# Kernel optimization log

Hardware: AMD Instinct MI355X
Metric: run time of the kernel (lower is better)

## Reference

```python
import jax, jax.numpy as jnp
import numpy as np
jax.config.update('jax_enable_x64', True)

N = 64
NX = N * N
BATCH = 32
EPS = 0.1
N_ITER = 25
SCHUR_REG = 1e-9
BIG = 1e10


def _constraints(group_ids, exposure):
    """Build shared equality system A z = b (doubly-stochastic + fairness row).
    Matches torch code which uses A = A[0] (first batch element only)."""
    ROW = jnp.kron(jnp.eye(N, dtype=jnp.float64), jnp.ones((1, N), dtype=jnp.float64))  # row sums
    COL = jnp.kron(jnp.ones((1, N), dtype=jnp.float64), jnp.eye(N, dtype=jnp.float64))  # col sums
    g = group_ids[0].astype(jnp.float64)                       # [N]
    f = g / g.sum() - (1.0 - g) / (1.0 - g).sum()              # group contrast
    fair = (f[:, None] * exposure.astype(jnp.float64)[None, :]).reshape(1, NX)  # entry i*N+j = f_i * expo_j
    A = jnp.concatenate([ROW, COL, fair], axis=0)              # [2N+1, NX]
    b = jnp.concatenate([jnp.ones(2 * N, dtype=jnp.float64), jnp.zeros(1, dtype=jnp.float64)])
    return A, b


def _solve_qp(p, A, b):
    """Batched primal-dual interior point for min 0.5*eps*||z||^2 + p'z
    s.t. A z = b, 0 <= z <= 1. G=[-I;I] structure is exploited: G'DG is diagonal,
    so each Newton step reduces to a small [neq,neq] Schur solve (as in qpth)."""
    B, nx = p.shape
    neq = A.shape[0]
    m = 2 * nx
    h = jnp.concatenate([jnp.zeros(nx, dtype=p.dtype), jnp.ones(nx, dtype=p.dtype)])
    eye_neq = jnp.eye(neq, dtype=p.dtype)

    def step(carry, _):
        z, y, s, lam = carry
        s1, s2 = s[:, :nx], s[:, nx:]
        l1, l2 = lam[:, :nx], lam[:, nx:]
        Gz = jnp.concatenate([-z, z], axis=1)
        r_dual = EPS * z + p + y @ A + (-l1 + l2)          # Qz + p + A'y + G'lam
        r_eq = z @ A.T - b                                  # A z - b
        r_ineq = Gz + s - h                                 # G z + s - h
        mu = jnp.sum(s * lam, axis=1, keepdims=True) / m
        r_cent = lam * s - 0.1 * mu                         # sigma = 0.1 centering
        tmp = (lam * r_ineq - r_cent) / s                   # [B, 2nx]
        rhs_z = -(r_dual + (-tmp[:, :nx] + tmp[:, nx:]))
        invD = 1.0 / (EPS + l1 / s1 + l2 / s2)              # (Q + G'DG)^{-1} diagonal
        S = jnp.einsum('ik,bk,jk->bij', A, invD, A) + SCHUR_REG * eye_neq
        rhs_y = (rhs_z * invD) @ A.T + r_eq
        dy = jnp.linalg.solve(S, rhs_y[..., None])[..., 0]
        dz = (rhs_z - dy @ A) * invD
        ds = -r_ineq - jnp.concatenate([-dz, dz], axis=1)
        dlam = (-r_cent - lam * ds) / s
        # fraction-to-boundary step length (grad-safe division)
        den_s = jnp.where(ds < 0, ds, -1.0)
        den_l = jnp.where(dlam < 0, dlam, -1.0)
        a_s = jnp.where(ds < 0, -s / den_s, BIG).min(axis=1)
        a_l = jnp.where(dlam < 0, -lam / den_l, BIG).min(axis=1)
        alpha = jnp.minimum(1.0, 0.99 * jnp.minimum(a_s, a_l))[:, None]
        return (z + alpha * dz, y + alpha * dy, s + alpha * ds, lam + alpha * dlam), None

    init = (jnp.zeros_like(p), jnp.zeros((B, neq), p.dtype),
            jnp.ones((B, m), p.dtype), jnp.ones((B, m), p.dtype))
    (z, _, _, _), _ = jax.lax.scan(step, init, None, length=N_ITER)
    return z


def setup_inputs() -> dict:
    key = jax.random.key(0)
    k1, k2 = jax.random.split(key)
    x = jax.random.normal(k1, (BATCH, NX), dtype=jnp.float32)
    gid = jax.random.randint(k2, (BATCH, N), 0, 2).astype(jnp.float32)
    # guarantee both groups present (avoid division by zero in f)
    gid = gid.at[:, 0].set(1.0).at[:, 1].set(0.0)
    exposure = (1.0 / jnp.log2(jnp.arange(N, dtype=jnp.float32) + 2.0))  # position_bias_vector[:N]
    return {"x": x, "group_ids": gid, "exposure": exposure}


def reference(x, group_ids, exposure):
    A, b = _constraints(group_ids, exposure)
    p = x.astype(jnp.float64)
    z = _solve_qp(p, A, b)
    return z.reshape(-1, N, N).astype(jnp.float32)
```

## Files before the change

kernel.cpp:

```cpp
#include <hip/hip_runtime.h>
#include <math.h>

#define NN    64
#define NXX   4096
#define NT    512
#define NCH   8
#define NITER 25
#define EPSQ  0.1
#define SREG  1e-9
#define BIGV  1e10

__device__ __forceinline__ double wsum(double v) {
#pragma unroll
  for (int m = 32; m > 0; m >>= 1) v += __shfl_xor(v, m, 64);
  return v;
}
__device__ __forceinline__ double wmin(double v) {
#pragma unroll
  for (int m = 32; m > 0; m >>= 1) v = fmin(v, __shfl_xor(v, m, 64));
  return v;
}
__device__ __forceinline__ double wmax(double v) {
#pragma unroll
  for (int m = 32; m > 0; m >>= 1) v = fmax(v, __shfl_xor(v, m, 64));
  return v;
}

__global__ __launch_bounds__(NT, 2)
void ipm_kernel(const float* __restrict__ xin, const float* __restrict__ gidin,
                const float* __restrict__ expin, float* __restrict__ outp)
{
  const int b    = blockIdx.x;
  const int tid  = threadIdx.x;
  const int lane = tid & 63;
  const int w    = tid >> 6;

  __shared__ double DnT[64][65];
  __shared__ double Mg[64][67];
  __shared__ double Pbuf[16][52];
  __shared__ double Binv[16][18];
  __shared__ double cpZ[8][64], cpA[8][64], cpB[8][64], cpC[8][64];
  __shared__ double rhs1[64], rhs2v[64];
  __shared__ double Rhv[64], Ruv[64], ccv[64], wvv[64];
  __shared__ double usv[64], rsv[64], uvv[64], mw0[64];
  __shared__ double ddv[64];
  __shared__ double yav[64], ydv[64];
  __shared__ double fvec[64], evec[64];
  __shared__ double wpFz[8], wpMu[8], wpQ[8], wpFg[8], wpS[8], wpL[8];
  __shared__ double scal[8];

  if (tid < 64) {
    fvec[tid] = (double)gidin[tid];
    evec[tid] = (double)expin[tid];
    yav[tid] = 0.0; ydv[tid] = 0.0;
  }
  if (tid == 0) scal[6] = 0.0;
  __syncthreads();
  if (tid == 0) {
    double gs = 0.0;
    for (int i = 0; i < 64; ++i) gs += fvec[i];
    scal[7] = gs;
  }
  __syncthreads();
  if (tid < 64) {
    double g = fvec[tid], gs = scal[7];
    fvec[tid] = g / gs - (1.0 - g) / (64.0 - gs);
  }
  __syncthreads();

  double p[NCH], z[NCH], s1[NCH], s2[NCH], l1[NCH], l2[NCH], fe[NCH];
  const double ev = evec[lane];
#pragma unroll
  for (int k = 0; k < NCH; ++k) {
    int e = tid + NT * k;
    p[k]  = (double)xin[(size_t)b * NXX + e];
    z[k] = 0.0; s1[k] = 1.0; s2[k] = 1.0; l1[k] = 1.0; l2[k] = 1.0;
    fe[k] = fvec[w + 8 * k] * ev;
  }

  for (int iter = 0; iter < NITER; ++iter) {
    double rq1[NCH];
    double cz = 0.0, fz = 0.0, msl = 0.0;
#pragma unroll
    for (int k = 0; k < NCH; ++k) {
      rq1[k] = wsum(z[k]) - 1.0;
      cz  += z[k];
      fz  += fe[k] * z[k];
      msl += s1[k] * l1[k] + s2[k] * l2[k];
    }
    cpZ[w][lane] = cz;
    {
      double a = wsum(fz), c = wsum(msl);
      if (lane == 0) { wpFz[w] = a; wpMu[w] = c; }
    }
    __syncthreads();

    double mu8 = 0.0;
#pragma unroll
    for (int q = 0; q < 8; ++q) mu8 += wpMu[q];
    const double mu01 = 0.1 * (mu8 / 8192.0);
    const double yt   = scal[6];
    double dinv[NCH], rz[NCH], is1[NCH], is2[NCH];
    double cD = 0.0, cfD = 0.0, cg = 0.0, qac = 0.0, fgac = 0.0;
#pragma unroll
    for (int k = 0; k < NCH; ++k) {
      int i = w + 8 * k;
      is1[k] = 1.0 / s1[k];  is2[k] = 1.0 / s2[k];
      double D = 1.0 / (EPSQ + l1[k] * is1[k] + l2[k] * is2[k]);
      dinv[k] = D;
      double rd  = EPSQ * z[k] + p[k] + (yav[i] + ydv[lane] + yt * fe[k]) + (l2[k] - l1[k]);
      double tt1 = (mu01 - l1[k] * z[k]) * is1[k];
      double tt2 = (l2[k] * (z[k] - 1.0) + mu01) * is2[k];
      double r = -(rd - tt1 + tt2);
      rz[k] = r;
      double g = r * D;
      double sD  = wsum(D);
      double sED = wsum(ev * D);
      double sg  = wsum(g);
      double Rh  = sD + SREG;
      if (lane == 0) {
        Rhv[i]  = Rh;
        Ruv[i]  = sED;
        rhs1[i] = sg + rq1[k];
      }
      DnT[lane][i] = D * rsqrt(Rh);
      cD  += D;  cfD += fvec[i] * D;  cg += g;
      qac += fe[k] * fe[k] * D;
      fgac += fe[k] * g;
    }
    cpA[w][lane] = cD; cpB[w][lane] = cfD; cpC[w][lane] = cg;
    {
      double a = wsum(qac), c = wsum(fgac);
      if (lane == 0) { wpQ[w] = a; wpFg[w] = c; }
    }
    __syncthreads();

    if (tid < 64) {
      double sZ = 0.0, sA = 0.0, sB = 0.0, sC = 0.0;
#pragma unroll
      for (int q = 0; q < 8; ++q) {
        sZ += cpZ[q][tid]; sA += cpA[q][tid]; sB += cpB[q][tid]; sC += cpC[q][tid];
      }
      ccv[tid]   = sA;
      wvv[tid]   = evec[tid] * sB;
      rhs2v[tid] = sC + sZ - 1.0;
      double ir  = rsqrt(Rhv[tid]);
      double u   = fvec[tid] * Ruv[tid];
      uvv[tid] = u;
      usv[tid] = u * ir;
      rsv[tid] = rhs1[tid] * ir;
    }
    __syncthreads();

    {
      const int r0 = (tid >> 5) << 2;
      const int c0 = (tid & 31) << 1;
      double m00=0.0,m01=0.0,m10=0.0,m11=0.0,m20=0.0,m21=0.0,m30=0.0,m31=0.0;
#pragma unroll 4
      for (int i = 0; i < 64; ++i) {
        double a0 = DnT[r0+0][i], a1 = DnT[r0+1][i];
        double a2 = DnT[r0+2][i], a3 = DnT[r0+3][i];
        double b0v = DnT[c0+0][i], b1v = DnT[c0+1][i];
        m00 += a0*b0v; m01 += a0*b1v;
        m10 += a1*b0v; m11 += a1*b1v;
        m20 += a2*b0v; m21 += a2*b1v;
        m30 += a3*b0v; m31 += a3*b1v;
      }
      Mg[r0+0][c0+0] = ((r0+0)==(c0+0) ? ccv[r0+0]+SREG : 0.0) - m00;
      Mg[r0+0][c0+1] = ((r0+0)==(c0+1) ? ccv[r0+0]+SREG : 0.0) - m01;
      Mg[r0+1][c0+0] = ((r0+1)==(c0+0) ? ccv[r0+1]+SREG : 0.0) - m10;
      Mg[r0+1][c0+1] = ((r0+1)==(c0+1) ? ccv[r0+1]+SREG : 0.0) - m11;
      Mg[r0+2][c0+0] = ((r0+2)==(c0+0) ? ccv[r0+2]+SREG : 0.0) - m20;
      Mg[r0+2][c0+1] = ((r0+2)==(c0+1) ? ccv[r0+2]+SREG : 0.0) - m21;
      Mg[r0+3][c0+0] = ((r0+3)==(c0+0) ? ccv[r0+3]+SREG : 0.0) - m30;
      Mg[r0+3][c0+1] = ((r0+3)==(c0+1) ? ccv[r0+3]+SREG : 0.0) - m31;

      int d = 16 * w + (lane >> 2);
      int j = d & 63;
      int cc = d >> 6;
      int iq = (lane & 3) * 16;
      double acc = 0.0;
#pragma unroll
      for (int i = 0; i < 16; ++i) {
        double vv = cc ? usv[iq + i] : rsv[iq + i];
        acc += DnT[j][iq + i] * vv;
      }
      acc += __shfl_xor(acc, 1, 64);
      acc += __shfl_xor(acc, 2, 64);
      if ((lane & 3) == 0) {
        if (cc == 0) Mg[j][64] = rhs2v[j] - acc;
        else { double vv2 = wvv[j] - acc; Mg[j][65] = vv2; mw0[j] = vv2; }
      }
    }
    __syncthreads();

#pragma unroll
    for (int pk = 0; pk < 4; ++pk) {
      const int k0   = 16 * pk;
      const int rest = 66 - k0 - 16;

      if (w == 0) {
        const int r = lane >> 2, q = lane & 3;
        double Brow[4];
#pragma unroll
        for (int e = 0; e < 4; ++e) Brow[e] = Mg[k0 + r][k0 + ((e << 2) | q)];
#pragma unroll
        for (int t = 0; t < 16; ++t) {
          const int et = t >> 2, qt = t & 3;
          double pm = __shfl(Brow[et], (r << 2) | qt, 64);
          double pv = __shfl(Brow[et], (t << 2) | qt, 64);
          double pr0 = __shfl(Brow[0], (t << 2) | q, 64);
          double pr1 = __shfl(Brow[1], (t << 2) | q, 64);
          double pr2 = __shfl(Brow[2], (t << 2) | q, 64);
          double pr3 = __shfl(Brow[3], (t << 2) | q, 64);
          double ip = 1.0 / pv;
          double ps0 = pr0 * ip, ps1 = pr1 * ip, ps2 = pr2 * ip, ps3 = pr3 * ip;
          if (r == t) {
            Brow[0] = ps0; Brow[1] = ps1; Brow[2] = ps2; Brow[3] = ps3;
            if (q == qt) Brow[et] = ip;
          } else {
            Brow[0] -= pm * ps0; Brow[1] -= pm * ps1;
            Brow[2] -= pm * ps2; Brow[3] -= pm * ps3;
            if (q == qt) Brow[et] = -pm * ip;
          }
        }
#pragma unroll
        for (int e = 0; e < 4; ++e) Binv[r][(e << 2) | q] = Brow[e];
      }
      __syncthreads();

      for (int o = tid; o < 16 * rest; o += NT) {
        int t = o / rest, c = o - t * rest;
        double acc = 0.0;
#pragma unroll
        for (int s = 0; s < 16; ++s) acc += Binv[t][s] * Mg[k0 + s][k0 + 16 + c];
        Pbuf[t][c] = acc;
      }
      __syncthreads();

      for (int o = tid; o < 48 * rest; o += NT) {
        int rr = o / rest, c = o - rr * rest;
        int r = rr < k0 ? rr : rr + 16;
        double acc = Mg[r][k0 + 16 + c];
#pragma unroll
        for (int t = 0; t < 16; ++t) acc -= Mg[r][k0 + t] * Pbuf[t][c];
        Mg[r][k0 + 16 + c] = acc;
      }
      for (int o = tid; o < 16 * rest; o += NT) {
        int t = o / rest, c = o - t * rest;
        Mg[k0 + t][k0 + 16 + c] = Pbuf[t][c];
      }
      __syncthreads();
    }

    if (w == 0) {
      double qsum = 0.0, fg = 0.0, fzs = 0.0;
#pragma unroll
      for (int q = 0; q < 8; ++q) { qsum += wpQ[q]; fg += wpFg[q]; fzs += wpFz[q]; }
      double h1 = Mg[lane][64], h2 = Mg[lane][65];
      double a1 = wsum(usv[lane] * usv[lane]);
      double a2 = wsum(usv[lane] * rsv[lane]);
      double a3 = wsum(mw0[lane] * h1);
      double a4 = wsum(mw0[lane] * h2);
      double qp  = qsum + SREG - a1;
      double r3p = (fg + fzs) - a2;
      double tloc = (r3p - a3) / (qp - a4);
      ddv[lane] = h1 - tloc * h2;
      if (lane == 0) scal[4] = tloc;
    }
    __syncthreads();

    const double tf = scal[4];
    double dar[NCH];
    double bs = 0.0;
    double rl = BIGV;
#pragma unroll
    for (int k = 0; k < NCH; ++k) {
      int i = w + 8 * k;
      double rdot = wsum(dinv[k] * ddv[lane]);
      double dv = (rhs1[i] - rdot - uvv[i] * tf) / Rhv[i];
      dar[k] = dv;
      double d   = (rz[k] - (dv + ddv[lane] + tf * fe[k])) * dinv[k];
      double ds1 = d - (s1[k] - z[k]);
      double ds2 = -(z[k] + s2[k] - 1.0) - d;
      bs = fmax(bs, fmax(-ds1 * is1[k], -ds2 * is2[k]));
      double dl1 = (-(l1[k] * s1[k] - mu01) - l1[k] * ds1) * is1[k];
      double dl2 = (-(l2[k] * s2[k] - mu01) - l2[k] * ds2) * is2[k];
      if (dl1 < 0.0) rl = fmin(rl, -l1[k] / dl1);
      if (dl2 < 0.0) rl = fmin(rl, -l2[k] / dl2);
    }
    bs = wmax(bs);
    rl = wmin(rl);
    if (lane == 0) { wpS[w] = bs; wpL[w] = rl; }
    __syncthreads();
    if (tid == 0) {
      double bm = wpS[0], rm = wpL[0];
      for (int q = 1; q < 8; ++q) { bm = fmax(bm, wpS[q]); rm = fmin(rm, wpL[q]); }
      double a_s = bm > 0.0 ? 1.0 / bm : BIGV;
      scal[5] = fmin(1.0, 0.99 * fmin(a_s, rm));
    }
    __syncthreads();

    const double al = scal[5];
#pragma unroll
    for (int k = 0; k < NCH; ++k) {
      double d   = (rz[k] - (dar[k] + ddv[lane] + tf * fe[k])) * dinv[k];
      double ds1 = d - (s1[k] - z[k]);
      double ds2 = -(z[k] + s2[k] - 1.0) - d;
      double dl1 = (-(l1[k] * s1[k] - mu01) - l1[k] * ds1) * is1[k];
      double dl2 = (-(l2[k] * s2[k] - mu01) - l2[k] * ds2) * is2[k];
      z[k]  += al * d;
      s1[k] += al * ds1;
      s2[k] += al * ds2;
      l1[k] += al * dl1;
      l2[k] += al * dl2;
      if (lane == 0) yav[w + 8 * k] += al * dar[k];
    }
    if (tid < 64) ydv[tid] += al * ddv[tid];
    if (tid == 0) scal[6] += al * tf;
  }

#pragma unroll
  for (int k = 0; k < NCH; ++k) {
    int e = tid + NT * k;
    outp[(size_t)b * NXX + e] = (float)z[k];
  }
}

extern "C" void kernel_launch(void* const* d_in, const int* in_sizes, int n_in,
                              void* d_out, int out_size, void* d_ws, size_t ws_size,
                              hipStream_t stream)
{
  const float* x   = (const float*)d_in[0];
  const float* gid = (const float*)d_in[1];
  const float* ex  = (const float*)d_in[2];
  float* out = (float*)d_out;
  int nb = in_sizes[0] / NXX;
  hipLaunchKernelGGL(ipm_kernel, dim3(nb), dim3(NT), 0, stream, x, gid, ex, out);
}
```

Before: 1.471 ms.

## Exploit Schur symmetry, overlap block inversion with trailing update, drop barriers

The Gram product is now computed only for upper-triangle tiles, and the lower triangle is mirrored afterward. Warp 0 inverts the next 16x16 pivot block using a Newton-refined hardware reciprocal, while the other warps update the remaining trailing matrix. This removes a barrier-separated inversion phase in each of the first three panel steps. The step-length and t-scalar computations are done redundantly in every warp instead of going through shared memory, which removes two more block barriers per iteration. The trade-offs are extra index arithmetic (sqrt-based pair decoding), load imbalance between warp 0 and the others, and slightly different reciprocal rounding.

```diff
diff --git a/kernel.cpp b/kernel.cpp
--- a/kernel.cpp
+++ b/kernel.cpp
@@ -26,6 +26,45 @@
   return v;
 }
 
+#define F1_INVERT(K0)                                                         \
+  {                                                                           \
+    const int r_ = lane >> 2, q_ = lane & 3;                                  \
+    double Brow[4];                                                           \
+    _Pragma("unroll")                                                         \
+    for (int e = 0; e < 4; ++e) Brow[e] = Mg[(K0) + r_][(K0) + ((e << 2) | q_)]; \
+    _Pragma("unroll")                                                         \
+    for (int t = 0; t < 16; ++t) {                                            \
+      const int et = t >> 2, qt = t & 3;                                      \
+      double pm  = __shfl(Brow[et], (r_ << 2) | qt, 64);                      \
+      double pv  = __shfl(Brow[et], (t << 2) | qt, 64);                       \
+      double pr0 = __shfl(Brow[0], (t << 2) | q_, 64);                        \
+      double pr1 = __shfl(Brow[1], (t << 2) | q_, 64);                        \
+      double pr2 = __shfl(Brow[2], (t << 2) | q_, 64);                        \
+      double pr3 = __shfl(Brow[3], (t << 2) | q_, 64);                        \
+      double ip = __builtin_amdgcn_rcp(pv);                                   \
+      ip = ip * (2.0 - pv * ip);                                              \
+      ip = ip * (2.0 - pv * ip);                                              \
+      double ps0 = pr0 * ip, ps1 = pr1 * ip, ps2 = pr2 * ip, ps3 = pr3 * ip;  \
+      if (r_ == t) {                                                          \
+        Brow[0] = ps0; Brow[1] = ps1; Brow[2] = ps2; Brow[3] = ps3;           \
+        if (q_ == qt) Brow[et] = ip;                                          \
+      } else {                                                                \
+        Brow[0] -= pm * ps0; Brow[1] -= pm * ps1;                             \
+        Brow[2] -= pm * ps2; Brow[3] -= pm * ps3;                             \
+        if (q_ == qt) Brow[et] = -pm * ip;                                    \
+      }                                                                       \
+    }                                                                         \
+    _Pragma("unroll")                                                         \
+    for (int e = 0; e < 4; ++e) Binv[r_][(e << 2) | q_] = Brow[e];            \
+  }
+
+__device__ __forceinline__ void pair_jl(int idx, int& j, int& l) {
+  j = (int)((1.0 + sqrt(8.0 * (double)idx + 1.0)) * 0.5);
+  while (j * (j - 1) / 2 > idx) --j;
+  while ((j + 1) * j / 2 <= idx) ++j;
+  l = idx - j * (j - 1) / 2;
+}
+
 __global__ __launch_bounds__(NT, 2)
 void ipm_kernel(const float* __restrict__ xin, const float* __restrict__ gidin,
                 const float* __restrict__ expin, float* __restrict__ outp)
@@ -43,7 +82,6 @@
   __shared__ double rhs1[64], rhs2v[64];
   __shared__ double Rhv[64], Ruv[64], ccv[64], wvv[64];
   __shared__ double usv[64], rsv[64], uvv[64], mw0[64];
-  __shared__ double ddv[64];
   __shared__ double yav[64], ydv[64];
   __shared__ double fvec[64], evec[64];
   __shared__ double wpFz[8], wpMu[8], wpQ[8], wpFg[8], wpS[8], wpL[8];
@@ -152,9 +190,12 @@
     }
     __syncthreads();
 
-    {
-      const int r0 = (tid >> 5) << 2;
-      const int c0 = (tid & 31) << 1;
+    if (tid < 272) {
+      int R = 0;
+#pragma unroll
+      for (int r = 1; r < 16; ++r) if (tid >= r * (33 - r)) R = r;
+      const int C  = 2 * R + (tid - R * (33 - R));
+      const int r0 = R << 2, c0 = C << 1;
       double m00=0.0,m01=0.0,m10=0.0,m11=0.0,m20=0.0,m21=0.0,m30=0.0,m31=0.0;
 #pragma unroll 4
       for (int i = 0; i < 64; ++i) {
@@ -174,22 +215,33 @@
       Mg[r0+2][c0+1] = ((r0+2)==(c0+1) ? ccv[r0+2]+SREG : 0.0) - m21;
       Mg[r0+3][c0+0] = ((r0+3)==(c0+0) ? ccv[r0+3]+SREG : 0.0) - m30;
       Mg[r0+3][c0+1] = ((r0+3)==(c0+1) ? ccv[r0+3]+SREG : 0.0) - m31;
-
-      int d = 16 * w + (lane >> 2);
-      int j = d & 63;
-      int cc = d >> 6;
-      int iq = (lane & 3) * 16;
+    } else if (tid < 400) {
+      const int d = tid - 272;
+      const int j = d & 63, cc = d >> 6;
       double acc = 0.0;
-#pragma unroll
-      for (int i = 0; i < 16; ++i) {
-        double vv = cc ? usv[iq + i] : rsv[iq + i];
-        acc += DnT[j][iq + i] * vv;
-      }
-      acc += __shfl_xor(acc, 1, 64);
-      acc += __shfl_xor(acc, 2, 64);
-      if ((lane & 3) == 0) {
-        if (cc == 0) Mg[j][64] = rhs2v[j] - acc;
-        else { double vv2 = wvv[j] - acc; Mg[j][65] = vv2; mw0[j] = vv2; }
+#pragma unroll 8
+      for (int i = 0; i < 64; ++i) {
+        double vv = cc ? usv[i] : rsv[i];
+        acc += DnT[j][i] * vv;
+      }
+      if (cc == 0) Mg[j][64] = rhs2v[j] - acc;
+      else { double vv2 = wvv[j] - acc; Mg[j][65] = vv2; mw0[j] = vv2; }
+    }
+    __syncthreads();
+
+    if (w == 0) {
+#pragma unroll
+      for (int e = 0; e < 2; ++e) {
+        int idx = 2 * lane + e;
+        if (idx < 120) { int j, l; pair_jl(idx, j, l); Mg[j][l] = Mg[l][j]; }
+      }
+      F1_INVERT(0);
+    } else {
+      const int wtid = tid - 64;
+#pragma unroll
+      for (int r = 0; r < 5; ++r) {
+        int idx = 120 + wtid + 448 * r;
+        if (idx < 2016) { int j, l; pair_jl(idx, j, l); Mg[j][l] = Mg[l][j]; }
       }
     }
     __syncthreads();
@@ -197,37 +249,7 @@
 #pragma unroll
     for (int pk = 0; pk < 4; ++pk) {
       const int k0   = 16 * pk;
-      const int rest = 66 - k0 - 16;
-
-      if (w == 0) {
-        const int r = lane >> 2, q = lane & 3;
-        double Brow[4];
-#pragma unroll
-        for (int e = 0; e < 4; ++e) Brow[e] = Mg[k0 + r][k0 + ((e << 2) | q)];
-#pragma unroll
-        for (int t = 0; t < 16; ++t) {
-          const int et = t >> 2, qt = t & 3;
-          double pm = __shfl(Brow[et], (r << 2) | qt, 64);
-          double pv = __shfl(Brow[et], (t << 2) | qt, 64);
-          double pr0 = __shfl(Brow[0], (t << 2) | q, 64);
-          double pr1 = __shfl(Brow[1], (t << 2) | q, 64);
-          double pr2 = __shfl(Brow[2], (t << 2) | q, 64);
-          double pr3 = __shfl(Brow[3], (t << 2) | q, 64);
-          double ip = 1.0 / pv;
-          double ps0 = pr0 * ip, ps1 = pr1 * ip, ps2 = pr2 * ip, ps3 = pr3 * ip;
-          if (r == t) {
-            Brow[0] = ps0; Brow[1] = ps1; Brow[2] = ps2; Brow[3] = ps3;
-            if (q == qt) Brow[et] = ip;
-          } else {
-            Brow[0] -= pm * ps0; Brow[1] -= pm * ps1;
-            Brow[2] -= pm * ps2; Brow[3] -= pm * ps3;
-            if (q == qt) Brow[et] = -pm * ip;
-          }
-        }
-#pragma unroll
-        for (int e = 0; e < 4; ++e) Binv[r][(e << 2) | q] = Brow[e];
-      }
-      __syncthreads();
+      const int rest = 50 - k0;
 
       for (int o = tid; o < 16 * rest; o += NT) {
         int t = o / rest, c = o - t * rest;
@@ -238,22 +260,55 @@
       }
       __syncthreads();
 
-      for (int o = tid; o < 48 * rest; o += NT) {
-        int rr = o / rest, c = o - rr * rest;
-        int r = rr < k0 ? rr : rr + 16;
-        double acc = Mg[r][k0 + 16 + c];
-#pragma unroll
-        for (int t = 0; t < 16; ++t) acc -= Mg[r][k0 + t] * Pbuf[t][c];
-        Mg[r][k0 + 16 + c] = acc;
-      }
-      for (int o = tid; o < 16 * rest; o += NT) {
-        int t = o / rest, c = o - t * rest;
-        Mg[k0 + t][k0 + 16 + c] = Pbuf[t][c];
+      if (pk < 3) {
+        if (w == 0) {
+#pragma unroll
+          for (int e = 0; e < 4; ++e) {
+            int idx = lane + 64 * e;
+            int r = k0 + 16 + (idx >> 4), c = (idx & 15);
+            double acc = Mg[r][k0 + 16 + c];
+#pragma unroll
+            for (int t = 0; t < 16; ++t) acc -= Mg[r][k0 + t] * Pbuf[t][c];
+            Mg[r][k0 + 16 + c] = acc;
+          }
+          F1_INVERT(k0 + 16);
+        } else {
+          const int wtid = tid - 64;
+          for (int o = wtid; o < 48 * rest; o += 448) {
+            int rr = o / rest, c = o - rr * rest;
+            int r = rr < k0 ? rr : rr + 16;
+            bool excl = (r >= k0 + 16) && (r < k0 + 32) && (c < 16);
+            if (!excl) {
+              double acc = Mg[r][k0 + 16 + c];
+#pragma unroll
+              for (int t = 0; t < 16; ++t) acc -= Mg[r][k0 + t] * Pbuf[t][c];
+              Mg[r][k0 + 16 + c] = acc;
+            }
+          }
+          for (int o = wtid; o < 16 * rest; o += 448) {
+            int t = o / rest, c = o - t * rest;
+            Mg[k0 + t][k0 + 16 + c] = Pbuf[t][c];
+          }
+        }
+      } else {
+        for (int o = tid; o < 48 * rest; o += NT) {
+          int rr = o / rest, c = o - rr * rest;
+          int r = rr < k0 ? rr : rr + 16;
+          double acc = Mg[r][k0 + 16 + c];
+#pragma unroll
+          for (int t = 0; t < 16; ++t) acc -= Mg[r][k0 + t] * Pbuf[t][c];
+          Mg[r][k0 + 16 + c] = acc;
+        }
+        for (int o = tid; o < 16 * rest; o += NT) {
+          int t = o / rest, c = o - t * rest;
+          Mg[k0 + t][k0 + 16 + c] = Pbuf[t][c];
+        }
       }
       __syncthreads();
     }
 
-    if (w == 0) {
+    double ddl, tf;
+    {
       double qsum = 0.0, fg = 0.0, fzs = 0.0;
 #pragma unroll
       for (int q = 0; q < 8; ++q) { qsum += wpQ[q]; fg += wpFg[q]; fzs += wpFz[q]; }
@@ -264,23 +319,20 @@
       double a4 = wsum(mw0[lane] * h2);
       double qp  = qsum + SREG - a1;
       double r3p = (fg + fzs) - a2;
-      double tloc = (r3p - a3) / (qp - a4);
-      ddv[lane] = h1 - tloc * h2;
-      if (lane == 0) scal[4] = tloc;
-    }
-    __syncthreads();
-
-    const double tf = scal[4];
+      tf  = (r3p - a3) / (qp - a4);
+      ddl = h1 - tf * h2;
+    }
+
     double dar[NCH];
     double bs = 0.0;
     double rl = BIGV;
 #pragma unroll
     for (int k = 0; k < NCH; ++k) {
       int i = w + 8 * k;
-      double rdot = wsum(dinv[k] * ddv[lane]);
+      double rdot = wsum(dinv[k] * ddl);
       double dv = (rhs1[i] - rdot - uvv[i] * tf) / Rhv[i];
       dar[k] = dv;
-      double d   = (rz[k] - (dv + ddv[lane] + tf * fe[k])) * dinv[k];
+      double d   = (rz[k] - (dv + ddl + tf * fe[k])) * dinv[k];
       double ds1 = d - (s1[k] - z[k]);
       double ds2 = -(z[k] + s2[k] - 1.0) - d;
       bs = fmax(bs, fmax(-ds1 * is1[k], -ds2 * is2[k]));
@@ -293,18 +345,18 @@
     rl = wmin(rl);
     if (lane == 0) { wpS[w] = bs; wpL[w] = rl; }
     __syncthreads();
-    if (tid == 0) {
+    double al;
+    {
       double bm = wpS[0], rm = wpL[0];
+#pragma unroll
       for (int q = 1; q < 8; ++q) { bm = fmax(bm, wpS[q]); rm = fmin(rm, wpL[q]); }
       double a_s = bm > 0.0 ? 1.0 / bm : BIGV;
-      scal[5] = fmin(1.0, 0.99 * fmin(a_s, rm));
-    }
-    __syncthreads();
-
-    const double al = scal[5];
+      al = fmin(1.0, 0.99 * fmin(a_s, rm));
+    }
+
 #pragma unroll
     for (int k = 0; k < NCH; ++k) {
-      double d   = (rz[k] - (dar[k] + ddv[lane] + tf * fe[k])) * dinv[k];
+      double d   = (rz[k] - (dar[k] + ddl + tf * fe[k])) * dinv[k];
       double ds1 = d - (s1[k] - z[k]);
       double ds2 = -(z[k] + s2[k] - 1.0) - d;
       double dl1 = (-(l1[k] * s1[k] - mu01) - l1[k] * ds1) * is1[k];
@@ -316,7 +368,7 @@
       l2[k] += al * dl2;
       if (lane == 0) yav[w + 8 * k] += al * dar[k];
     }
-    if (tid < 64) ydv[tid] += al * ddv[tid];
+    if (tid < 64) ydv[tid] += al * ddl;
     if (tid == 0) scal[6] += al * tf;
   }
 
```

Result: faster. 1.295 ms (-12.0%).
